# Optimization experiments

Measured on AMD Instinct MI355X. Metric: run time of the kernel, lower is better.

The kernel has to match this reference:

```python
import jax, jax.numpy as jnp
import numpy as np

H = 8           # hidden_size
IN = 1          # input_size
OUT = 1         # output_size
T_IN = 512      # input_length
T_OUT = 128     # output_length
B = 65536       # batch


def _gru_cell(x, h, W_ih, W_hh, b_ih, b_hh):
    # torch.nn.GRUCell math. x: [B, D], h: [B, H]
    gi = x @ W_ih.T + b_ih          # [B, 3H]
    gh = h @ W_hh.T + b_hh          # [B, 3H]
    i_r, i_z, i_n = jnp.split(gi, 3, axis=-1)
    h_r, h_z, h_n = jnp.split(gh, 3, axis=-1)
    r = jax.nn.sigmoid(i_r + h_r)
    z = jax.nn.sigmoid(i_z + h_z)
    n = jnp.tanh(i_n + r * h_n)
    return (1.0 - z) * n + z * h


def setup_inputs() -> dict:
    key = jax.random.key(0)
    ks = jax.random.split(key, 12)
    s_in = 1.0 / np.sqrt(H)
    x = jax.random.normal(ks[0], (T_IN, B, IN), dtype=jnp.float32)
    u = lambda k, shp: jax.random.uniform(k, shp, dtype=jnp.float32, minval=-s_in, maxval=s_in)
    return {
        "x": x,
        "enc_W_ih": u(ks[1], (3 * H, IN)),
        "enc_W_hh": u(ks[2], (3 * H, H)),
        "enc_b_ih": u(ks[3], (3 * H,)),
        "enc_b_hh": u(ks[4], (3 * H,)),
        "dec_W_ih": u(ks[5], (3 * H, OUT)),
        "dec_W_hh": u(ks[6], (3 * H, H)),
        "dec_b_ih": u(ks[7], (3 * H,)),
        "dec_b_hh": u(ks[8], (3 * H,)),
        "fc_W": u(ks[9], (OUT, H)),
        "fc_b": u(ks[10], (OUT,)),
    }


def reference(x, enc_W_ih, enc_W_hh, enc_b_ih, enc_b_hh,
              dec_W_ih, dec_W_hh, dec_b_ih, dec_b_hh, fc_W, fc_b):
    batch = x.shape[1]
    h0 = jnp.zeros((batch, H), dtype=x.dtype)

    def enc_step(h, x_t):
        return _gru_cell(x_t, h, enc_W_ih, enc_W_hh, enc_b_ih, enc_b_hh), None

    enc_h, _ = jax.lax.scan(enc_step, h0, x)

    def dec_step(carry, _):
        h, inp = carry
        h = _gru_cell(inp, h, dec_W_ih, dec_W_hh, dec_b_ih, dec_b_hh)
        out_t = h @ fc_W.T + fc_b      # [B, OUT]
        return (h, out_t), out_t

    # decoder_feat is None, teacher_forcing False: feed back own prediction
    _, outs = jax.lax.scan(dec_step, (enc_h, x[-1]), None, length=T_OUT)
    return outs  # [T_OUT, B, OUT]
```

## Files before the change

### kernel.cpp

```cpp
#include <hip/hip_runtime.h>

#define T_IN   512
#define T_OUT  128
#define BATCH  65536

typedef float v2f __attribute__((ext_vector_type(2)));

__device__ __forceinline__ float exp2_fast(float v) { return __builtin_amdgcn_exp2f(v); }
__device__ __forceinline__ float rcp_fast(float v)  { return __builtin_amdgcn_rcpf(v); }

__device__ __forceinline__ v2f pk_fma(v2f a, v2f b, v2f c) {
    v2f d;
    asm("v_pk_fma_f32 %0, %1, %2, %3" : "=v"(d) : "v"(a), "v"(b), "v"(c));
    return d;
}

template<int CTRL>
__device__ __forceinline__ float dppf(float v) {
    return __int_as_float(__builtin_amdgcn_mov_dpp(__float_as_int(v), CTRL, 0xF, 0xF, false));
}
#define QP_XOR1 0xB1
#define QP_XOR2 0x4E
#define QP_XOR3 0x1B
#define HALF_MIRROR 0x141

__global__ __launch_bounds__(256, 4) void gru_seq2seq(
    const float* __restrict__ x,
    const float* __restrict__ eWih, const float* __restrict__ eWhh,
    const float* __restrict__ eBih, const float* __restrict__ eBhh,
    const float* __restrict__ dWih, const float* __restrict__ dWhh,
    const float* __restrict__ dBih, const float* __restrict__ dBhh,
    const float* __restrict__ fcW,  const float* __restrict__ fcB,
    float* __restrict__ out)
{
    const int tid = threadIdx.x;
    const int u   = tid & 7;
    const int e0  = (int)blockIdx.x * 64 + (tid >> 3);
    const int e1  = e0 + 32;

    const float CR = -1.44269504088896340736f;
    const float CN =  2.88539008177792681472f;

    v2f wr[4], wz[4], wn[4];
    v2f brv, bzv, bnv;
    float wir, wiz, win, binS;

    auto load_w = [&](const float* Wih, const float* Whh,
                      const float* Bih, const float* Bhh) {
        #pragma unroll
        for (int p = 0; p < 4; ++p) {
            const int c0 = u ^ (2*p), c1 = u ^ (2*p + 1);
            wr[p] = v2f{ Whh[u*8      + c0] * CR, Whh[u*8      + c1] * CR };
            wz[p] = v2f{ Whh[(u+8)*8  + c0] * CR, Whh[(u+8)*8  + c1] * CR };
            wn[p] = v2f{ Whh[(u+16)*8 + c0] * CN, Whh[(u+16)*8 + c1] * CN };
        }
        wir = Wih[u]    * CR;  wiz = Wih[u+8] * CR;  win = Wih[u+16] * CN;
        brv = v2f{ (Bih[u]   + Bhh[u])   * CR, 0.f };
        bzv = v2f{ (Bih[u+8] + Bhh[u+8]) * CR, 0.f };
        bnv = v2f{ Bhh[u+16] * CN,             0.f };
        binS = Bih[u+16] * CN;
    };

    load_w(eWih, eWhh, eBih, eBhh);

    float h[2] = {0.f, 0.f};
    v2f h01[2] = {{0.f,0.f},{0.f,0.f}}, h23[2] = {{0.f,0.f},{0.f,0.f}};
    v2f h45[2] = {{0.f,0.f},{0.f,0.f}}, h67[2] = {{0.f,0.f},{0.f,0.f}};

    auto cell = [&](int i, float xin) {
        v2f ar = pk_fma(wr[0], h01[i], brv);
        v2f az = pk_fma(wz[0], h01[i], bzv);
        v2f an = pk_fma(wn[0], h01[i], bnv);
        ar = pk_fma(wr[1], h23[i], ar);
        az = pk_fma(wz[1], h23[i], az);
        an = pk_fma(wn[1], h23[i], an);
        ar = pk_fma(wr[2], h45[i], ar);
        az = pk_fma(wz[2], h45[i], az);
        an = pk_fma(wn[2], h45[i], an);
        ar = pk_fma(wr[3], h67[i], ar);
        az = pk_fma(wz[3], h67[i], az);
        an = pk_fma(wn[3], h67[i], an);

        const float sr = fmaf(xin, wir, ar.x + ar.y);
        const float sz = fmaf(xin, wiz, az.x + az.y);
        const float hn = an.x + an.y;

        const float er = exp2_fast(sr);
        const float ez = exp2_fast(sz);
        const float dr = 1.0f + er;
        const float dz = 1.0f + ez;
        const float rp = rcp_fast(dr * dz);
        const float r  = dz * rp;
        const float z  = dr * rp;

        float pre = fmaf(xin, win, binS);
        pre = fmaf(r, hn, pre);
        const float en = exp2_fast(pre);
        const float rn = rcp_fast(1.0f + en);
        const float n  = fmaf(-2.0f, rn, 1.0f);

        h[i] = fmaf(z, h[i] - n, n);

        const float hh = h[i];
        h01[i].x = hh;
        h01[i].y = dppf<QP_XOR1>(hh);
        h23[i].x = dppf<QP_XOR2>(hh);
        h23[i].y = dppf<QP_XOR1>(h23[i].x);
        h67[i].y = dppf<HALF_MIRROR>(hh);
        h67[i].x = dppf<QP_XOR1>(h67[i].y);
        h45[i].y = dppf<QP_XOR2>(h67[i].y);
        h45[i].x = dppf<QP_XOR3>(h67[i].y);
    };

    const float* xp = x + e0;
    float xa0 = xp[0],     xb0 = xp[32];
    float xa1 = xp[BATCH], xb1 = xp[BATCH + 32];
    xp += 2 * (size_t)BATCH;
    #pragma unroll 2
    for (int t = 0; t < T_IN - 2; ++t) {
        const float xa2 = xp[0];
        const float xb2 = xp[32];
        xp += BATCH;
        cell(0, xa0);
        cell(1, xb0);
        xa0 = xa1; xa1 = xa2;
        xb0 = xb1; xb1 = xb2;
    }
    cell(0, xa0); cell(1, xb0);
    cell(0, xa1); cell(1, xb1);

    load_w(dWih, dWhh, dBih, dBhh);
    v2f fw[4];
    #pragma unroll
    for (int p = 0; p < 4; ++p)
        fw[p] = v2f{ fcW[u ^ (2*p)], fcW[u ^ (2*p + 1)] };
    const v2f fbv = v2f{ fcB[0], 0.f };

    float inp0 = xa1, inp1 = xb1;
    float* outp = out + e0;
    #pragma unroll 1
    for (int t = 0; t < T_OUT; ++t) {
        cell(0, inp0);
        cell(1, inp1);
        v2f ay0 = pk_fma(fw[0], h01[0], fbv);
        v2f ay1 = pk_fma(fw[0], h01[1], fbv);
        ay0 = pk_fma(fw[1], h23[0], ay0);
        ay1 = pk_fma(fw[1], h23[1], ay1);
        ay0 = pk_fma(fw[2], h45[0], ay0);
        ay1 = pk_fma(fw[2], h45[1], ay1);
        ay0 = pk_fma(fw[3], h67[0], ay0);
        ay1 = pk_fma(fw[3], h67[1], ay1);
        const float y0 = ay0.x + ay0.y;
        const float y1 = ay1.x + ay1.y;
        if (u == 0) {
            outp[t * BATCH]      = y0;
            outp[t * BATCH + 32] = y1;
        }
        inp0 = y0;
        inp1 = y1;
    }
}

extern "C" void kernel_launch(void* const* d_in, const int* in_sizes, int n_in,
                              void* d_out, int out_size, void* d_ws, size_t ws_size,
                              hipStream_t stream) {
    const float* x    = (const float*)d_in[0];
    const float* eWih = (const float*)d_in[1];
    const float* eWhh = (const float*)d_in[2];
    const float* eBih = (const float*)d_in[3];
    const float* eBhh = (const float*)d_in[4];
    const float* dWih = (const float*)d_in[5];
    const float* dWhh = (const float*)d_in[6];
    const float* dBih = (const float*)d_in[7];
    const float* dBhh = (const float*)d_in[8];
    const float* fcW  = (const float*)d_in[9];
    const float* fcB  = (const float*)d_in[10];
    float* out = (float*)d_out;

    dim3 grid(BATCH / 64);
    dim3 block(256);
    gru_seq2seq<<<grid, block, 0, stream>>>(x, eWih, eWhh, eBih, eBhh,
                                            dWih, dWhh, dBih, dBhh,
                                            fcW, fcB, out);
}
```

Baseline: 430.3 us.

## Pack two batch elements per packed-FMA lane instead of splitting hidden dims

Result: faster. 382.5 us (-11.1%).

```diff
diff --git a/kernel.cpp b/kernel.cpp
--- a/kernel.cpp
+++ b/kernel.cpp
@@ -36,128 +36,120 @@
     const int tid = threadIdx.x;
     const int u   = tid & 7;
     const int e0  = (int)blockIdx.x * 64 + (tid >> 3);
-    const int e1  = e0 + 32;
 
     const float CR = -1.44269504088896340736f;
     const float CN =  2.88539008177792681472f;
 
-    v2f wr[4], wz[4], wn[4];
-    v2f brv, bzv, bnv;
-    float wir, wiz, win, binS;
+    v2f wr[8], wz[8], wn[8];
+    v2f wirv, wizv, winv;
+    v2f brv, bzv, bnv, binv;
+
+    auto dup = [](float v) { return v2f{v, v}; };
 
     auto load_w = [&](const float* Wih, const float* Whh,
                       const float* Bih, const float* Bhh) {
         #pragma unroll
-        for (int p = 0; p < 4; ++p) {
-            const int c0 = u ^ (2*p), c1 = u ^ (2*p + 1);
-            wr[p] = v2f{ Whh[u*8      + c0] * CR, Whh[u*8      + c1] * CR };
-            wz[p] = v2f{ Whh[(u+8)*8  + c0] * CR, Whh[(u+8)*8  + c1] * CR };
-            wn[p] = v2f{ Whh[(u+16)*8 + c0] * CN, Whh[(u+16)*8 + c1] * CN };
+        for (int d = 0; d < 8; ++d) {
+            const int c = u ^ d;
+            wr[d] = dup(Whh[u*8      + c] * CR);
+            wz[d] = dup(Whh[(u+8)*8  + c] * CR);
+            wn[d] = dup(Whh[(u+16)*8 + c] * CN);
         }
-        wir = Wih[u]    * CR;  wiz = Wih[u+8] * CR;  win = Wih[u+16] * CN;
-        brv = v2f{ (Bih[u]   + Bhh[u])   * CR, 0.f };
-        bzv = v2f{ (Bih[u+8] + Bhh[u+8]) * CR, 0.f };
-        bnv = v2f{ Bhh[u+16] * CN,             0.f };
-        binS = Bih[u+16] * CN;
+        wirv = dup(Wih[u]    * CR);
+        wizv = dup(Wih[u+8]  * CR);
+        winv = dup(Wih[u+16] * CN);
+        brv  = dup((Bih[u]   + Bhh[u])   * CR);
+        bzv  = dup((Bih[u+8] + Bhh[u+8]) * CR);
+        bnv  = dup(Bhh[u+16] * CN);
+        binv = dup(Bih[u+16] * CN);
     };
 
     load_w(eWih, eWhh, eBih, eBhh);
 
-    float h[2] = {0.f, 0.f};
-    v2f h01[2] = {{0.f,0.f},{0.f,0.f}}, h23[2] = {{0.f,0.f},{0.f,0.f}};
-    v2f h45[2] = {{0.f,0.f},{0.f,0.f}}, h67[2] = {{0.f,0.f},{0.f,0.f}};
+    const v2f C_NEG2 = {-2.f, -2.f};
+    const v2f C_ONE  = { 1.f,  1.f};
 
-    auto cell = [&](int i, float xin) {
-        v2f ar = pk_fma(wr[0], h01[i], brv);
-        v2f az = pk_fma(wz[0], h01[i], bzv);
-        v2f an = pk_fma(wn[0], h01[i], bnv);
-        ar = pk_fma(wr[1], h23[i], ar);
-        az = pk_fma(wz[1], h23[i], az);
-        an = pk_fma(wn[1], h23[i], an);
-        ar = pk_fma(wr[2], h45[i], ar);
-        az = pk_fma(wz[2], h45[i], az);
-        an = pk_fma(wn[2], h45[i], an);
-        ar = pk_fma(wr[3], h67[i], ar);
-        az = pk_fma(wz[3], h67[i], az);
-        an = pk_fma(wn[3], h67[i], an);
+    v2f hp[8];
+    #pragma unroll
+    for (int d = 0; d < 8; ++d) hp[d] = v2f{0.f, 0.f};
 
-        const float sr = fmaf(xin, wir, ar.x + ar.y);
-        const float sz = fmaf(xin, wiz, az.x + az.y);
-        const float hn = an.x + an.y;
+    auto cell2 = [&](v2f xp) {
+        v2f ar = brv, az = bzv, an = bnv;
+        #pragma unroll
+        for (int d = 0; d < 8; ++d) {
+            ar = pk_fma(wr[d], hp[d], ar);
+            az = pk_fma(wz[d], hp[d], az);
+            an = pk_fma(wn[d], hp[d], an);
+        }
+        const v2f sr = pk_fma(xp, wirv, ar);
+        const v2f sz = pk_fma(xp, wizv, az);
 
-        const float er = exp2_fast(sr);
-        const float ez = exp2_fast(sz);
-        const float dr = 1.0f + er;
-        const float dz = 1.0f + ez;
-        const float rp = rcp_fast(dr * dz);
-        const float r  = dz * rp;
-        const float z  = dr * rp;
+        const float er0 = exp2_fast(sr.x), er1 = exp2_fast(sr.y);
+        const float ez0 = exp2_fast(sz.x), ez1 = exp2_fast(sz.y);
+        const float dr0 = 1.0f + er0, dr1 = 1.0f + er1;
+        const float dz0 = 1.0f + ez0, dz1 = 1.0f + ez1;
+        const float P0  = dr0 * dz0,  P1  = dr1 * dz1;
+        const float rp  = rcp_fast(P0 * P1);
+        const float rpA = rp * P1,    rpB = rp * P0;
+        const v2f r01 = { dz0 * rpA, dz1 * rpB };
+        const v2f z01 = { dr0 * rpA, dr1 * rpB };
 
-        float pre = fmaf(xin, win, binS);
-        pre = fmaf(r, hn, pre);
-        const float en = exp2_fast(pre);
-        const float rn = rcp_fast(1.0f + en);
-        const float n  = fmaf(-2.0f, rn, 1.0f);
+        v2f pre = pk_fma(xp, winv, binv);
+        pre = pk_fma(r01, an, pre);
+        const float en0 = exp2_fast(pre.x), en1 = exp2_fast(pre.y);
+        const float Dn0 = 1.0f + en0, Dn1 = 1.0f + en1;
+        const float rpn = rcp_fast(Dn0 * Dn1);
+        const v2f rn  = { rpn * Dn1, rpn * Dn0 };
+        const v2f n01 = pk_fma(C_NEG2, rn, C_ONE);
 
-        h[i] = fmaf(z, h[i] - n, n);
+        const v2f hm = hp[0] - n01;
+        hp[0] = pk_fma(z01, hm, n01);
 
-        const float hh = h[i];
-        h01[i].x = hh;
-        h01[i].y = dppf<QP_XOR1>(hh);
-        h23[i].x = dppf<QP_XOR2>(hh);
-        h23[i].y = dppf<QP_XOR1>(h23[i].x);
-        h67[i].y = dppf<HALF_MIRROR>(hh);
-        h67[i].x = dppf<QP_XOR1>(h67[i].y);
-        h45[i].y = dppf<QP_XOR2>(h67[i].y);
-        h45[i].x = dppf<QP_XOR3>(h67[i].y);
+        const float g0 = hp[0].x, g1 = hp[0].y;
+        float a7x = dppf<HALF_MIRROR>(g0);
+        float a7y = dppf<HALF_MIRROR>(g1);
+        hp[1] = v2f{ dppf<QP_XOR1>(g0), dppf<QP_XOR1>(g1) };
+        hp[2] = v2f{ dppf<QP_XOR2>(g0), dppf<QP_XOR2>(g1) };
+        hp[3] = v2f{ dppf<QP_XOR3>(g0), dppf<QP_XOR3>(g1) };
+        hp[7] = v2f{ a7x, a7y };
+        hp[6] = v2f{ dppf<QP_XOR1>(a7x), dppf<QP_XOR1>(a7y) };
+        hp[5] = v2f{ dppf<QP_XOR2>(a7x), dppf<QP_XOR2>(a7y) };
+        hp[4] = v2f{ dppf<QP_XOR3>(a7x), dppf<QP_XOR3>(a7y) };
     };
 
     const float* xp = x + e0;
-    float xa0 = xp[0],     xb0 = xp[32];
-    float xa1 = xp[BATCH], xb1 = xp[BATCH + 32];
+    v2f xa0 = { xp[0],     xp[32] };
+    v2f xa1 = { xp[BATCH], xp[BATCH + 32] };
     xp += 2 * (size_t)BATCH;
     #pragma unroll 2
     for (int t = 0; t < T_IN - 2; ++t) {
-        const float xa2 = xp[0];
-        const float xb2 = xp[32];
+        const v2f xa2 = { xp[0], xp[32] };
         xp += BATCH;
-        cell(0, xa0);
-        cell(1, xb0);
+        cell2(xa0);
         xa0 = xa1; xa1 = xa2;
-        xb0 = xb1; xb1 = xb2;
     }
-    cell(0, xa0); cell(1, xb0);
-    cell(0, xa1); cell(1, xb1);
+    cell2(xa0);
+    cell2(xa1);
 
     load_w(dWih, dWhh, dBih, dBhh);
-    v2f fw[4];
+    v2f fw[8];
     #pragma unroll
-    for (int p = 0; p < 4; ++p)
-        fw[p] = v2f{ fcW[u ^ (2*p)], fcW[u ^ (2*p + 1)] };
-    const v2f fbv = v2f{ fcB[0], 0.f };
+    for (int d = 0; d < 8; ++d) fw[d] = dup(fcW[u ^ d]);
+    const v2f fbv = dup(fcB[0]);
 
-    float inp0 = xa1, inp1 = xb1;
+    v2f inp = xa1;
     float* outp = out + e0;
     #pragma unroll 1
     for (int t = 0; t < T_OUT; ++t) {
-        cell(0, inp0);
-        cell(1, inp1);
-        v2f ay0 = pk_fma(fw[0], h01[0], fbv);
-        v2f ay1 = pk_fma(fw[0], h01[1], fbv);
-        ay0 = pk_fma(fw[1], h23[0], ay0);
-        ay1 = pk_fma(fw[1], h23[1], ay1);
-        ay0 = pk_fma(fw[2], h45[0], ay0);
-        ay1 = pk_fma(fw[2], h45[1], ay1);
-        ay0 = pk_fma(fw[3], h67[0], ay0);
-        ay1 = pk_fma(fw[3], h67[1], ay1);
-        const float y0 = ay0.x + ay0.y;
-        const float y1 = ay1.x + ay1.y;
+        cell2(inp);
+        v2f ay = fbv;
+        #pragma unroll
+        for (int d = 0; d < 8; ++d) ay = pk_fma(fw[d], hp[d], ay);
         if (u == 0) {
-            outp[t * BATCH]      = y0;
-            outp[t * BATCH + 32] = y1;
+            outp[t * BATCH]      = ay.x;
+            outp[t * BATCH + 32] = ay.y;
         }
-        inp0 = y0;
-        inp1 = y1;
+        inp = ay;
     }
 }
 
```
